# Kernel optimization log

Measured on AMD Instinct MI355X. Metric: run time of the kernel, lower is better.

Reference implementation:

```python
import jax, jax.numpy as jnp
import numpy as np

NUM_NODES = 2048   # N (spatial)
SEQ_LEN = 512      # T (temporal)
LATENT = 32
LAYERS = 2
SELF_LOOP_EPS = 0.5
B = 4


def setup_inputs() -> dict:
    key = jax.random.key(0)
    k1, k2, k3 = jax.random.split(key, 3)
    NT = NUM_NODES + SEQ_LEN
    X = jax.random.normal(k1, (B, NT, LATENT), dtype=jnp.float32)
    # GraphSAGE-style per-layer weights: self and neighbor transforms + bias
    Ws = jax.random.normal(k2, (LAYERS, LATENT, LATENT), dtype=jnp.float32) * 0.05
    Wn = jax.random.normal(k3, (LAYERS, LATENT, LATENT), dtype=jnp.float32) * 0.05
    b = jnp.zeros((LAYERS, LATENT), dtype=jnp.float32)
    return {"X": X, "Ws": Ws, "Wn": Wn, "b": b}


def build_adj(X):
    # node_embs = concat(spatial, temporal) == X itself
    adj = jnp.einsum('bnf,bmf->bnm', X, X)          # [B, N+T, N+T]
    adj = jnp.tanh(jax.nn.relu(adj))
    NT = X.shape[1]
    adj = adj + SELF_LOOP_EPS * jnp.eye(NT, dtype=adj.dtype)
    return adj


def reference(X, Ws, Wn, b):
    adj = build_adj(X)
    h = X
    # dense weighted aggregation == sparse message passing over nonzero edges,
    # since edge weights are exactly the adjacency values
    for l in range(LAYERS):
        agg = jnp.einsum('bnm,bmd->bnd', adj, h)    # neighbor aggregation
        h = jax.nn.elu(jnp.einsum('bnd,de->bne', h, Ws[l])
                       + jnp.einsum('bnd,de->bne', agg, Wn[l])
                       + b[l])
    return h
```

## Files before the change

kernel.cpp:

```cpp
#include <hip/hip_runtime.h>
#include <math.h>

#define NT 2560
#define DF 32
#define NB 4
#define SELF_EPS 0.5f
#define MS 8
#define MROWS (NT / MS)
#define MT 64
#define MITERS (MROWS / MT)
#define TN 64

typedef __attribute__((ext_vector_type(8))) short bf16x8;
typedef __attribute__((ext_vector_type(4))) float f32x4;

__device__ __forceinline__ unsigned short f2bf(float f) {
    unsigned u = __builtin_bit_cast(unsigned, f);
    u += 0x7fffu + ((u >> 16) & 1u);
    return (unsigned short)(u >> 16);
}

__device__ __forceinline__ float fast_rcp(float x) {
#if __has_builtin(__builtin_amdgcn_rcpf)
    return __builtin_amdgcn_rcpf(x);
#else
    return 1.0f / x;
#endif
}

__device__ __forceinline__ float tanh_relu(float x) {
    x = fmaxf(x, 0.0f);
    float e = __expf(x + x);
    return 1.0f - 2.0f * fast_rcp(e + 1.0f);
}

__global__ __launch_bounds__(256, 4)
void prep(const float* __restrict__ X,
          unsigned short* __restrict__ Xb, unsigned short* __restrict__ XT)
{
    const int t = threadIdx.x;
    __shared__ float sT[32][33];
    const int tile = blockIdx.x;
    const int b = tile / 80, n0 = (tile % 80) * 32;
    const int row = t >> 3, c4 = (t & 7) * 4;
    const size_t rbase = ((size_t)(b * NT + n0 + row)) * DF + c4;
    const float4 v = *(const float4*)(X + rbase);
    unsigned p0 = (unsigned)f2bf(v.x) | ((unsigned)f2bf(v.y) << 16);
    unsigned p1 = (unsigned)f2bf(v.z) | ((unsigned)f2bf(v.w) << 16);
    *(uint2*)(Xb + rbase) = make_uint2(p0, p1);
    sT[row][c4 + 0] = v.x; sT[row][c4 + 1] = v.y;
    sT[row][c4 + 2] = v.z; sT[row][c4 + 3] = v.w;
    __syncthreads();
    const int d = t >> 3, nq = (t & 7) * 4;
    unsigned q0 = (unsigned)f2bf(sT[nq + 0][d]) | ((unsigned)f2bf(sT[nq + 1][d]) << 16);
    unsigned q1 = (unsigned)f2bf(sT[nq + 2][d]) | ((unsigned)f2bf(sT[nq + 3][d]) << 16);
    *(uint2*)(XT + ((size_t)(b * DF + d)) * NT + n0 + nq) = make_uint2(q0, q1);
}

__global__ __launch_bounds__(256, 4)
void gsage_main(const unsigned short* __restrict__ Xb,
                const unsigned short* __restrict__ HT,
                float* __restrict__ P)
{
    __shared__ unsigned short XmL[64 * 40];
    __shared__ unsigned short HtL[32 * 72];
    __shared__ unsigned short Ss[4 * 16 * 72];

    const int t = threadIdx.x;
    const int w = t >> 6, lane = t & 63;
    const int q = lane >> 4, c = lane & 15;
    const int n0 = blockIdx.x * TN;
    const int mbase = blockIdx.y * MROWS;
    const int b = blockIdx.z;

    const size_t xbase = (size_t)b * NT * DF;
    const size_t tbase = (size_t)b * DF * NT;

    const bf16x8 bfn = *(const bf16x8*)(Xb + xbase + (size_t)(n0 + w * 16 + c) * DF + q * 8);

    f32x4 acc0 = {0.f, 0.f, 0.f, 0.f};
    f32x4 acc1 = {0.f, 0.f, 0.f, 0.f};

    const int xrow = t >> 2, xseg = t & 3;
    const int hrow = t >> 3, hseg = t & 7;

    uint4 xv = *(const uint4*)(Xb + xbase + (size_t)(mbase + xrow) * DF + xseg * 8);
    uint4 hv = *(const uint4*)(HT + tbase + (size_t)hrow * NT + mbase + hseg * 8);

    const int n_g = n0 + w * 16 + c;
    unsigned short* SsW = Ss + w * (16 * 72);

    for (int it = 0; it < MITERS; ++it) {
        const int m0 = mbase + it * MT;
        __syncthreads();
        *(uint4*)(XmL + xrow * 40 + xseg * 8) = xv;
        *(uint4*)(HtL + hrow * 72 + hseg * 8) = hv;
        if (it + 1 < MITERS) {
            const int m1 = m0 + MT;
            xv = *(const uint4*)(Xb + xbase + (size_t)(m1 + xrow) * DF + xseg * 8);
            hv = *(const uint4*)(HT + tbase + (size_t)hrow * NT + m1 + hseg * 8);
        }
        __syncthreads();

        if (m0 == n0) {
            #pragma unroll
            for (int t4 = 0; t4 < 4; ++t4) {
                const bf16x8 af = *(const bf16x8*)(XmL + (t4 * 16 + c) * 40 + q * 8);
                const f32x4 zero = {0.f, 0.f, 0.f, 0.f};
                f32x4 st = __builtin_amdgcn_mfma_f32_16x16x32_bf16(af, bfn, zero, 0, 0, 0);
                const int m2 = m0 + t4 * 16 + q * 4;
                float v0 = tanh_relu(st[0]); if (n_g == m2 + 0) v0 += SELF_EPS;
                float v1 = tanh_relu(st[1]); if (n_g == m2 + 1) v1 += SELF_EPS;
                float v2 = tanh_relu(st[2]); if (n_g == m2 + 2) v2 += SELF_EPS;
                float v3 = tanh_relu(st[3]); if (n_g == m2 + 3) v3 += SELF_EPS;
                unsigned p0 = (unsigned)f2bf(v0) | ((unsigned)f2bf(v1) << 16);
                unsigned p1 = (unsigned)f2bf(v2) | ((unsigned)f2bf(v3) << 16);
                *(uint2*)(SsW + c * 72 + t4 * 16 + q * 4) = make_uint2(p0, p1);
            }
        } else {
            #pragma unroll
            for (int t4 = 0; t4 < 4; ++t4) {
                const bf16x8 af = *(const bf16x8*)(XmL + (t4 * 16 + c) * 40 + q * 8);
                const f32x4 zero = {0.f, 0.f, 0.f, 0.f};
                f32x4 st = __builtin_amdgcn_mfma_f32_16x16x32_bf16(af, bfn, zero, 0, 0, 0);
                float v0 = tanh_relu(st[0]);
                float v1 = tanh_relu(st[1]);
                float v2 = tanh_relu(st[2]);
                float v3 = tanh_relu(st[3]);
                unsigned p0 = (unsigned)f2bf(v0) | ((unsigned)f2bf(v1) << 16);
                unsigned p1 = (unsigned)f2bf(v2) | ((unsigned)f2bf(v3) << 16);
                *(uint2*)(SsW + c * 72 + t4 * 16 + q * 4) = make_uint2(p0, p1);
            }
        }
        asm volatile("s_waitcnt lgkmcnt(0)" ::: "memory");

        #pragma unroll
        for (int kc = 0; kc < 2; ++kc) {
            const bf16x8 sf = *(const bf16x8*)(SsW + c * 72 + kc * 32 + q * 8);
            const bf16x8 h0 = *(const bf16x8*)(HtL + c * 72 + kc * 32 + q * 8);
            const bf16x8 h1 = *(const bf16x8*)(HtL + (16 + c) * 72 + kc * 32 + q * 8);
            acc0 = __builtin_amdgcn_mfma_f32_16x16x32_bf16(sf, h0, acc0, 0, 0, 0);
            acc1 = __builtin_amdgcn_mfma_f32_16x16x32_bf16(sf, h1, acc1, 0, 0, 0);
        }
    }

    float* ap = P + ((size_t)blockIdx.y * NB + b) * NT * DF
                  + (size_t)(n0 + w * 16 + q * 4) * DF + c;
    #pragma unroll
    for (int r = 0; r < 4; ++r) {
        ap[(size_t)r * DF] = acc0[r];
        ap[(size_t)r * DF + 16] = acc1[r];
    }
}

__global__ __launch_bounds__(256, 4)
void gsage_epi(const float* __restrict__ Hin, const float* __restrict__ P,
               const float* __restrict__ Wsl, const float* __restrict__ Wnl,
               const float* __restrict__ bl,
               float* __restrict__ Hout, unsigned short* __restrict__ HTout)
{
    __shared__ float sW[32][33], sN[32][33], sH[32][36], sA[32][36], sT[32][33];
    const int t = threadIdx.x;
    const int n0 = blockIdx.x * 32;
    const int b = blockIdx.y;
    const int row = t >> 3, c4 = (t & 7) * 4;
    const size_t rb = ((size_t)(b * NT + n0 + row)) * DF + c4;
    const float4 hv = *(const float4*)(Hin + rb);
    const size_t pstride = (size_t)NB * NT * DF;
    float4 av = *(const float4*)(P + rb);
    #pragma unroll
    for (int s = 1; s < MS; ++s) {
        const float4 pv = *(const float4*)(P + (size_t)s * pstride + rb);
        av.x += pv.x; av.y += pv.y; av.z += pv.z; av.w += pv.w;
    }
    const float4 w0 = *(const float4*)(Wsl + row * DF + c4);
    const float4 w1 = *(const float4*)(Wnl + row * DF + c4);
    sH[row][c4+0]=hv.x; sH[row][c4+1]=hv.y; sH[row][c4+2]=hv.z; sH[row][c4+3]=hv.w;
    sA[row][c4+0]=av.x; sA[row][c4+1]=av.y; sA[row][c4+2]=av.z; sA[row][c4+3]=av.w;
    sW[row][c4+0]=w0.x; sW[row][c4+1]=w0.y; sW[row][c4+2]=w0.z; sW[row][c4+3]=w0.w;
    sN[row][c4+0]=w1.x; sN[row][c4+1]=w1.y; sN[row][c4+2]=w1.z; sN[row][c4+3]=w1.w;
    __syncthreads();

    float4 z = make_float4(bl[c4+0], bl[c4+1], bl[c4+2], bl[c4+3]);
    #pragma unroll
    for (int k = 0; k < DF; ++k) {
        const float hk = sH[row][k], ak = sA[row][k];
        z.x += hk * sW[k][c4+0] + ak * sN[k][c4+0];
        z.y += hk * sW[k][c4+1] + ak * sN[k][c4+1];
        z.z += hk * sW[k][c4+2] + ak * sN[k][c4+2];
        z.w += hk * sW[k][c4+3] + ak * sN[k][c4+3];
    }
    z.x = z.x > 0.f ? z.x : __expf(z.x) - 1.f;
    z.y = z.y > 0.f ? z.y : __expf(z.y) - 1.f;
    z.z = z.z > 0.f ? z.z : __expf(z.z) - 1.f;
    z.w = z.w > 0.f ? z.w : __expf(z.w) - 1.f;
    *(float4*)(Hout + rb) = z;

    if (HTout != nullptr) {
        sT[row][c4+0]=z.x; sT[row][c4+1]=z.y; sT[row][c4+2]=z.z; sT[row][c4+3]=z.w;
        __syncthreads();
        const int d = t >> 3, nq = (t & 7) * 4;
        unsigned q0 = (unsigned)f2bf(sT[nq+0][d]) | ((unsigned)f2bf(sT[nq+1][d]) << 16);
        unsigned q1 = (unsigned)f2bf(sT[nq+2][d]) | ((unsigned)f2bf(sT[nq+3][d]) << 16);
        *(uint2*)(HTout + ((size_t)(b * DF + d)) * NT + n0 + nq) = make_uint2(q0, q1);
    }
}

extern "C" void kernel_launch(void* const* d_in, const int* in_sizes, int n_in,
                              void* d_out, int out_size, void* d_ws, size_t ws_size,
                              hipStream_t stream) {
    const float* X  = (const float*)d_in[0];
    const float* Ws = (const float*)d_in[1];
    const float* Wn = (const float*)d_in[2];
    const float* bv = (const float*)d_in[3];
    float* out = (float*)d_out;

    char* ws = (char*)d_ws;
    float* P  = (float*)ws;
    float* h1 = P + (size_t)MS * NB * NT * DF;
    unsigned short* Xb  = (unsigned short*)(ws + 11796480);
    unsigned short* XT  = Xb + (size_t)NB * NT * DF;
    unsigned short* H1T = XT + (size_t)NB * NT * DF;

    prep<<<320, 256, 0, stream>>>(X, Xb, XT);

    dim3 g(NT / TN, MS, NB);
    gsage_main<<<g, 256, 0, stream>>>(Xb, XT, P);
    gsage_epi<<<dim3(NT / 32, NB), 256, 0, stream>>>(X, P, Ws, Wn, bv, h1, H1T);
    gsage_main<<<g, 256, 0, stream>>>(Xb, H1T, P);
    gsage_epi<<<dim3(NT / 32, NB), 256, 0, stream>>>(h1, P, Ws + DF * DF, Wn + DF * DF,
                                                     bv + DF, out, nullptr);
}
```

Before: 106.4 us.

## Materialize bf16 adjacency in layer one and reuse it in layer two

The first aggregation kernel now also writes every tanh(relu(X·Xᵀ)) adjacency fragment to a global scratch buffer, stored in bf16 and in MFMA-operand order. A new gsage_agg kernel for the second layer streams those fragments back in, prefetching the next iteration's fragments, and only does the adjacency-times-H MFMAs. This removes the second round of Gram-matrix MFMAs and tanh evaluation. In exchange it adds about 50 MB of global writes in layer one and the same volume of reads in layer two, and it relies on the workspace being large enough for the extra buffer.

```diff
diff --git a/kernel.cpp b/kernel.cpp
--- a/kernel.cpp
+++ b/kernel.cpp
@@ -10,6 +10,7 @@
 #define MT 64
 #define MITERS (MROWS / MT)
 #define TN 64
+#define NBK (NT / TN)
 
 typedef __attribute__((ext_vector_type(8))) short bf16x8;
 typedef __attribute__((ext_vector_type(4))) float f32x4;
@@ -60,7 +61,8 @@
 __global__ __launch_bounds__(256, 4)
 void gsage_main(const unsigned short* __restrict__ Xb,
                 const unsigned short* __restrict__ HT,
-                float* __restrict__ P)
+                float* __restrict__ P,
+                unsigned short* __restrict__ Sg)
 {
     __shared__ unsigned short XmL[64 * 40];
     __shared__ unsigned short HtL[32 * 72];
@@ -89,6 +91,11 @@
 
     const int n_g = n0 + w * 16 + c;
     unsigned short* SsW = Ss + w * (16 * 72);
+
+    unsigned short* Sgw = Sg
+        + ((((size_t)b * MS + blockIdx.y) * NBK + blockIdx.x) * 4 + w)
+          * ((size_t)MITERS * 2 * 64 * 8)
+        + (size_t)lane * 8;
 
     for (int it = 0; it < MITERS; ++it) {
         const int m0 = mbase + it * MT;
@@ -137,11 +144,74 @@
         #pragma unroll
         for (int kc = 0; kc < 2; ++kc) {
             const bf16x8 sf = *(const bf16x8*)(SsW + c * 72 + kc * 32 + q * 8);
+            *(uint4*)(Sgw + (size_t)(it * 2 + kc) * (64 * 8)) = __builtin_bit_cast(uint4, sf);
             const bf16x8 h0 = *(const bf16x8*)(HtL + c * 72 + kc * 32 + q * 8);
             const bf16x8 h1 = *(const bf16x8*)(HtL + (16 + c) * 72 + kc * 32 + q * 8);
             acc0 = __builtin_amdgcn_mfma_f32_16x16x32_bf16(sf, h0, acc0, 0, 0, 0);
             acc1 = __builtin_amdgcn_mfma_f32_16x16x32_bf16(sf, h1, acc1, 0, 0, 0);
         }
+    }
+
+    float* ap = P + ((size_t)blockIdx.y * NB + b) * NT * DF
+                  + (size_t)(n0 + w * 16 + q * 4) * DF + c;
+    #pragma unroll
+    for (int r = 0; r < 4; ++r) {
+        ap[(size_t)r * DF] = acc0[r];
+        ap[(size_t)r * DF + 16] = acc1[r];
+    }
+}
+
+__global__ __launch_bounds__(256, 6)
+void gsage_agg(const unsigned short* __restrict__ Sg,
+               const unsigned short* __restrict__ HT,
+               float* __restrict__ P)
+{
+    __shared__ unsigned short HtL[32 * 72];
+
+    const int t = threadIdx.x;
+    const int w = t >> 6, lane = t & 63;
+    const int q = lane >> 4, c = lane & 15;
+    const int n0 = blockIdx.x * TN;
+    const int mbase = blockIdx.y * MROWS;
+    const int b = blockIdx.z;
+    const size_t tbase = (size_t)b * DF * NT;
+
+    const int hrow = t >> 3, hseg = t & 7;
+    uint4 hv = *(const uint4*)(HT + tbase + (size_t)hrow * NT + mbase + hseg * 8);
+
+    const unsigned short* Sp = Sg
+        + ((((size_t)b * MS + blockIdx.y) * NBK + blockIdx.x) * 4 + w)
+          * ((size_t)MITERS * 2 * 64 * 8)
+        + (size_t)lane * 8;
+
+    bf16x8 sf0 = *(const bf16x8*)(Sp);
+    bf16x8 sf1 = *(const bf16x8*)(Sp + 64 * 8);
+
+    f32x4 acc0 = {0.f, 0.f, 0.f, 0.f};
+    f32x4 acc1 = {0.f, 0.f, 0.f, 0.f};
+
+    for (int it = 0; it < MITERS; ++it) {
+        __syncthreads();
+        *(uint4*)(HtL + hrow * 72 + hseg * 8) = hv;
+        bf16x8 nsf0, nsf1;
+        if (it + 1 < MITERS) {
+            hv = *(const uint4*)(HT + tbase + (size_t)hrow * NT
+                                 + (mbase + (it + 1) * MT) + hseg * 8);
+            nsf0 = *(const bf16x8*)(Sp + (size_t)((it + 1) * 2 + 0) * (64 * 8));
+            nsf1 = *(const bf16x8*)(Sp + (size_t)((it + 1) * 2 + 1) * (64 * 8));
+        }
+        __syncthreads();
+
+        const bf16x8 h00 = *(const bf16x8*)(HtL + c * 72 + 0 * 32 + q * 8);
+        const bf16x8 h01 = *(const bf16x8*)(HtL + (16 + c) * 72 + 0 * 32 + q * 8);
+        acc0 = __builtin_amdgcn_mfma_f32_16x16x32_bf16(sf0, h00, acc0, 0, 0, 0);
+        acc1 = __builtin_amdgcn_mfma_f32_16x16x32_bf16(sf0, h01, acc1, 0, 0, 0);
+        const bf16x8 h10 = *(const bf16x8*)(HtL + c * 72 + 1 * 32 + q * 8);
+        const bf16x8 h11 = *(const bf16x8*)(HtL + (16 + c) * 72 + 1 * 32 + q * 8);
+        acc0 = __builtin_amdgcn_mfma_f32_16x16x32_bf16(sf1, h10, acc0, 0, 0, 0);
+        acc1 = __builtin_amdgcn_mfma_f32_16x16x32_bf16(sf1, h11, acc1, 0, 0, 0);
+
+        if (it + 1 < MITERS) { sf0 = nsf0; sf1 = nsf1; }
     }
 
     float* ap = P + ((size_t)blockIdx.y * NB + b) * NT * DF
@@ -221,13 +291,14 @@
     unsigned short* Xb  = (unsigned short*)(ws + 11796480);
     unsigned short* XT  = Xb + (size_t)NB * NT * DF;
     unsigned short* H1T = XT + (size_t)NB * NT * DF;
+    unsigned short* Sg  = H1T + (size_t)NB * NT * DF;
 
     prep<<<320, 256, 0, stream>>>(X, Xb, XT);
 
-    dim3 g(NT / TN, MS, NB);
-    gsage_main<<<g, 256, 0, stream>>>(Xb, XT, P);
+    dim3 g(NBK, MS, NB);
+    gsage_main<<<g, 256, 0, stream>>>(Xb, XT, P, Sg);
     gsage_epi<<<dim3(NT / 32, NB), 256, 0, stream>>>(X, P, Ws, Wn, bv, h1, H1T);
-    gsage_main<<<g, 256, 0, stream>>>(Xb, H1T, P);
+    gsage_agg<<<g, 256, 0, stream>>>(Sg, H1T, P);
     gsage_epi<<<dim3(NT / 32, NB), 256, 0, stream>>>(h1, P, Ws + DF * DF, Wn + DF * DF,
                                                      bv + DF, out, nullptr);
 }
```

Measured after the change: 100.7 us. 1.06x faster.
